# Kernel optimization log

Measured on AMD Instinct MI355X. Metric: run time of the kernel, lower is better.

The kernel has to match this reference:

```python
import jax, jax.numpy as jnp
import numpy as np


def setup_inputs() -> dict:
    key = jax.random.key(0)
    ks = jax.random.split(key, 8)
    B, N, D = 8, 2048, 128
    s = 1.0 / float(np.sqrt(D))
    node = jax.random.normal(ks[0], (B, N, D), dtype=jnp.float32)
    node_mask = jax.random.randint(ks[1], (B, N), 0, 2, dtype=jnp.int32)
    punctuation_graph = jax.random.randint(ks[2], (B, N, N), 0, 2, dtype=jnp.int32)
    w_nw = jax.random.uniform(ks[3], (1, D), jnp.float32, -s, s)
    b_nw = jax.random.uniform(ks[4], (1,), jnp.float32, -s, s)
    w_self = jax.random.uniform(ks[5], (D, D), jnp.float32, -s, s)
    b_self = jax.random.uniform(ks[6], (D,), jnp.float32, -s, s)
    w_punct = jax.random.uniform(ks[7], (D, D), jnp.float32, -s, s)
    return {"node": node, "node_mask": node_mask, "punctuation_graph": punctuation_graph,
            "w_nw": w_nw, "b_nw": b_nw, "w_self": w_self, "b_self": b_self,
            "w_punct": w_punct, "iteration_steps": 2}


def reference(node, node_mask, punctuation_graph, w_nw, b_nw, w_self, b_self, w_punct, iteration_steps):
    B, N, D = node.shape
    # dd_graph = mask outer product with zeroed diagonal; graph = dd_graph * punctuation_graph
    eye = jnp.eye(N, dtype=punctuation_graph.dtype)
    dd = node_mask[:, None, :] * node_mask[:, :, None] * (1 - eye)[None, :, :]  # [B,N,N]
    graph = dd * punctuation_graph  # [B,N,N] int, binary
    nbr_num = graph.sum(-1)  # [B,N]
    # replace_masked_values(nbr_num, nbr_num>=1, 1): nodes with no neighbors get denom 1
    nbr_f = jnp.where(nbr_num >= 1, nbr_num.astype(node.dtype), jnp.asarray(1.0, node.dtype))
    gmask = graph > 0
    weights = []
    x = node
    for _ in range(iteration_steps):  # small fixed step count
        dw = jax.nn.sigmoid(jnp.einsum('bnd,od->bno', x, w_nw) + b_nw)[..., 0]  # [B,N]
        weights.append(dw)
        self_info = jnp.einsum('bnd,ed->bne', x, w_self) + b_self  # [B,N,D]
        info_p = jnp.einsum('bnd,ed->bne', x, w_punct)  # [B,N,D]
        # node_weight[b,i,j] = dw[b,j] where graph[b,i,j] else 0
        nw = jnp.where(gmask, dw[:, None, :], jnp.asarray(0.0, x.dtype))  # [B,N,N]
        agg = jnp.einsum('bnm,bmd->bnd', nw, info_p) / nbr_f[..., None]
        x = jax.nn.relu(self_info + agg)
    all_weight = jnp.stack(weights, axis=1)  # [B, steps, N]
    return x, all_weight
```

## Files before the change

### kernel.cpp

```cpp
#include <hip/hip_runtime.h>
#include <hip/hip_bf16.h>

#define BB 8
#define NN 2048
#define DD 128

typedef __attribute__((ext_vector_type(8))) __bf16 bf16x8;
typedef __attribute__((ext_vector_type(4))) float f32x4;
typedef __attribute__((ext_vector_type(4))) int   i32x4;

static __device__ __forceinline__ unsigned short f2bf(float f) {
    union { float f; unsigned u; } v; v.f = f;
    unsigned r = (v.u + 0x7FFFu + ((v.u >> 16) & 1u)) >> 16;
    return (unsigned short)r;
}
static __device__ __forceinline__ float bf2f(unsigned short b) {
    union { unsigned u; float f; } v; v.u = ((unsigned)b) << 16;
    return v.f;
}

__global__ __launch_bounds__(256) void kernP3(
    const int* __restrict__ punct, const int* __restrict__ mask,
    const float* __restrict__ w_self, const float* __restrict__ w_punct,
    unsigned* __restrict__ pk, float* __restrict__ scale_g, float* __restrict__ pdm_g,
    unsigned short* __restrict__ wsb, unsigned short* __restrict__ wpb)
{
    const int bid = blockIdx.x;
    const int t = threadIdx.x;

    if (bid >= 2048) {
        const int cb = bid - 2048;
        const float* src = (cb < 8) ? w_self : w_punct;
        unsigned short* dst = (cb < 8) ? wsb : wpb;
        const size_t i0 = (size_t)(cb & 7) * 2048 + (size_t)t * 8;
        f32x4 a = *(const f32x4*)(src + i0);
        f32x4 c = *(const f32x4*)(src + i0 + 4);
        unsigned q0 = f2bf(a.x) | ((unsigned)f2bf(a.y) << 16);
        unsigned q1 = f2bf(a.z) | ((unsigned)f2bf(a.w) << 16);
        unsigned q2 = f2bf(c.x) | ((unsigned)f2bf(c.y) << 16);
        unsigned q3 = f2bf(c.z) | ((unsigned)f2bf(c.w) << 16);
        i32x4 pw = {(int)q0, (int)q1, (int)q2, (int)q3};
        *(i32x4*)(dst + i0) = pw;
        return;
    }

    const int wave = t >> 6, lane = t & 63;
    const int row0 = bid * 8 + wave * 2;
    const int b = row0 >> 11;
    const int* mrow = mask + (size_t)b * NN;

    unsigned mw = 0;
    #pragma unroll
    for (int q = 0; q < 8; ++q) {
        i32x4 m = *(const i32x4*)(mrow + lane * 32 + q * 4);
        unsigned nib = (m.x & 1) | ((m.y & 1) << 1) | ((m.z & 1) << 2) | ((m.w & 1) << 3);
        mw |= nib << (4 * q);
    }

    #pragma unroll
    for (int r = 0; r < 2; ++r) {
        const int row = row0 + r;
        const int i = row & (NN - 1);
        const int mi = mrow[i];
        if (mi == 0) {
            if (lane == 0) { scale_g[row] = 0.f; pdm_g[row] = 0.f; }
            continue;
        }
        const int* prow = punct + (size_t)row * NN;
        i32x4 v[8];
        #pragma unroll
        for (int q = 0; q < 8; ++q)
            v[q] = *(const i32x4*)(prow + lane * 32 + q * 4);
        unsigned wd = 0;
        #pragma unroll
        for (int q = 0; q < 8; ++q) {
            unsigned nib = (v[q].x & 1) | ((v[q].y & 1) << 1)
                         | ((v[q].z & 1) << 2) | ((v[q].w & 1) << 3);
            wd |= nib << (4 * q);
        }
        wd &= mw;
        pk[(size_t)row * 64 + lane] = wd;

        int acc = __popc(wd);
        if ((i >> 5) == lane) acc += (int)((wd >> (i & 31)) & 1u) << 16;
        #pragma unroll
        for (int o = 32; o > 0; o >>= 1) acc += __shfl_xor(acc, o, 64);
        if (lane == 0) {
            const int nall = acc & 0xFFFF;
            const int pd   = acc >> 16;
            const int nbr  = nall - pd;
            scale_g[row] = 1.f / (float)(nbr < 1 ? 1 : nbr);
            pdm_g[row]   = (float)pd;
        }
    }
}

static __device__ __forceinline__ void kernB_body(
    int n0, const float* __restrict__ x,
    const float* __restrict__ w_nw,  const float* __restrict__ b_nw,
    const unsigned short* __restrict__ wsb, const float* __restrict__ b_self,
    const unsigned short* __restrict__ wpb,
    const float* __restrict__ scale_g, const float* __restrict__ pdm_g,
    float* __restrict__ si_out,
    unsigned short* __restrict__ yT_out,
    float* __restrict__ aw_out)
{
    __shared__ unsigned short xt[64*32];
    __shared__ unsigned short wst[128*32];
    __shared__ unsigned short wpt[128*32];
    __shared__ float wnw_l[DD];
    __shared__ float red[256];
    __shared__ float dw_l[64];
    __shared__ float scl_l[64];
    __shared__ float pdm_l[64];
    __shared__ unsigned short ytl[128*72];

    const int t  = threadIdx.x;
    const int b  = n0 >> 11;
    const int nb = n0 & (NN - 1);

    if (t < DD) wnw_l[t] = w_nw[t];
    if (t >= 128 && t < 192) { scl_l[t-128] = scale_g[n0 + t - 128]; }
    if (t >= 192)            { pdm_l[t-192] = pdm_g[n0 + t - 192]; }
    __syncthreads();

    const int wave = t >> 6, lane = t & 63;
    const int wm = wave >> 1, wn = wave & 1;
    const int quad = lane >> 4, l16 = lane & 15;

    const int n_loc = t >> 2, dq = t & 3;
    const int we = t >> 1,   wh = t & 1;

    f32x4 accs[2][4] = {}; f32x4 accp[2][4] = {};
    float dwpart = 0.f;

    #pragma unroll
    for (int kk = 0; kk < 4; ++kk) {
        const int k0 = kk * 32;
        {
            const float* xs = x + (size_t)(n0 + n_loc) * DD + k0 + dq * 8;
            f32x4 a = *(const f32x4*)xs;
            f32x4 c = *(const f32x4*)(xs + 4);
            const float* wv = &wnw_l[k0 + dq * 8];
            dwpart += a.x*wv[0] + a.y*wv[1] + a.z*wv[2] + a.w*wv[3]
                    + c.x*wv[4] + c.y*wv[5] + c.z*wv[6] + c.w*wv[7];
            unsigned q0 = f2bf(a.x) | ((unsigned)f2bf(a.y) << 16);
            unsigned q1 = f2bf(a.z) | ((unsigned)f2bf(a.w) << 16);
            unsigned q2 = f2bf(c.x) | ((unsigned)f2bf(c.y) << 16);
            unsigned q3 = f2bf(c.z) | ((unsigned)f2bf(c.w) << 16);
            i32x4 pw = {(int)q0,(int)q1,(int)q2,(int)q3};
            *(i32x4*)&xt[n_loc*32 + dq*8] = pw;
        }
        {
            const unsigned short* s1 = wsb + (size_t)we * DD + k0 + wh*16;
            const unsigned short* s2 = wpb + (size_t)we * DD + k0 + wh*16;
            i32x4 a0 = *(const i32x4*)s1;
            i32x4 a1 = *(const i32x4*)(s1 + 8);
            *(i32x4*)&wst[we*32 + wh*16]     = a0;
            *(i32x4*)&wst[we*32 + wh*16 + 8] = a1;
            i32x4 c0 = *(const i32x4*)s2;
            i32x4 c1 = *(const i32x4*)(s2 + 8);
            *(i32x4*)&wpt[we*32 + wh*16]     = c0;
            *(i32x4*)&wpt[we*32 + wh*16 + 8] = c1;
        }
        __syncthreads();
        bf16x8 af[2], bs[4], bp[4];
        #pragma unroll
        for (int mt = 0; mt < 2; ++mt)
            af[mt] = *(const bf16x8*)&xt[(wm*32 + mt*16 + l16)*32 + quad*8];
        #pragma unroll
        for (int nt = 0; nt < 4; ++nt) {
            const int er = wn*64 + nt*16 + l16;
            bs[nt] = *(const bf16x8*)&wst[er*32 + quad*8];
            bp[nt] = *(const bf16x8*)&wpt[er*32 + quad*8];
        }
        #pragma unroll
        for (int mt = 0; mt < 2; ++mt)
            #pragma unroll
            for (int nt = 0; nt < 4; ++nt) {
                accs[mt][nt] = __builtin_amdgcn_mfma_f32_16x16x32_bf16(af[mt], bs[nt], accs[mt][nt], 0, 0, 0);
                accp[mt][nt] = __builtin_amdgcn_mfma_f32_16x16x32_bf16(af[mt], bp[nt], accp[mt][nt], 0, 0, 0);
            }
        __syncthreads();
    }

    red[t] = dwpart;
    __syncthreads();
    if (t < 64) {
        float s = red[4*t] + red[4*t+1] + red[4*t+2] + red[4*t+3] + b_nw[0];
        float dv = 1.f / (1.f + __expf(-s));
        dw_l[t] = dv;
        aw_out[(size_t)b * 2 * NN + nb + t] = dv;
    }
    __syncthreads();

    #pragma unroll
    for (int mt = 0; mt < 2; ++mt) {
        #pragma unroll
        for (int nt = 0; nt < 4; ++nt) {
            const int e = wn*64 + nt*16 + l16;
            const float bsv = b_self[e];
            #pragma unroll
            for (int r = 0; r < 4; ++r) {
                const int nl = wm*32 + mt*16 + quad*4 + r;
                const size_t idx = (size_t)(n0 + nl) * DD + e;
                const float yv = dw_l[nl] * accp[mt][nt][r];
                const unsigned short ub = f2bf(yv);
                const float yvr = bf2f(ub);
                si_out[idx] = accs[mt][nt][r] + bsv - scl_l[nl] * pdm_l[nl] * yvr;
                ytl[e*72 + nl] = ub;
            }
        }
    }
    __syncthreads();
    {
        const int e = t >> 1, half = t & 1;
        const i32x4* src = (const i32x4*)&ytl[e*72 + half*32];
        i32x4 v0 = src[0], v1 = src[1], v2 = src[2], v3 = src[3];
        i32x4* dst = (i32x4*)(yT_out + (size_t)(b*DD + e) * NN + nb + half*32);
        dst[0] = v0; dst[1] = v1; dst[2] = v2; dst[3] = v3;
    }
}

__global__ __launch_bounds__(256) void kernB(
    const float* __restrict__ x,
    const unsigned short* __restrict__ wsb, const unsigned short* __restrict__ wpb,
    const float* __restrict__ w_nw, const float* __restrict__ b_nw,
    const float* __restrict__ b_self,
    const float* __restrict__ scale_g, const float* __restrict__ pdm_g,
    float* __restrict__ si, unsigned short* __restrict__ yT,
    float* __restrict__ aw_s)
{
    kernB_body(blockIdx.x * 64, x, w_nw, b_nw, wsb, b_self, wpb,
               scale_g, pdm_g, si, yT, aw_s);
}

__global__ __launch_bounds__(256) void kernC4(
    const unsigned* __restrict__ pk,
    const float* __restrict__ scale_g,
    const unsigned short* __restrict__ yT,
    const float* __restrict__ sip,
    float* __restrict__ x_out)
{
    __shared__ unsigned pPk[64 * 68];
    __shared__ float scale_l[64];
    __shared__ f32x4 accL[2][16][64];

    const int t  = threadIdx.x;
    const int b  = blockIdx.x & 7;
    const int i0 = (blockIdx.x >> 3) * 64;
    const size_t rg0 = (size_t)b * NN + i0;

    #pragma unroll
    for (int r = 0; r < 4; ++r) {
        const int u   = r * 256 + t;
        const int row = u >> 4;
        const int wq  = (u & 15) * 4;
        i32x4 v = *(const i32x4*)(pk + (rg0 + row) * 64 + wq);
        *(i32x4*)&pPk[row * 68 + wq] = v;
    }
    if (t < 64) scale_l[t] = scale_g[rg0 + t];
    __syncthreads();

    const int wave = t >> 6, lane = t & 63;
    const int kh = wave >> 1, eh = wave & 1;
    const int quad = lane >> 4, l16 = lane & 15;
    const unsigned short* yTb = yT + (size_t)b * DD * NN;

    f32x4 acc[4][4] = {};

    #pragma unroll 4
    for (int ks = 0; ks < 32; ++ks) {
        const int kk = kh * 32 + ks;
        bf16x8 bfr[4];
        #pragma unroll
        for (int nt = 0; nt < 4; ++nt) {
            const int e = eh*64 + nt*16 + l16;
            bfr[nt] = *(const bf16x8*)(yTb + (size_t)e * NN + kk*32 + quad*8);
        }
        bf16x8 af[4];
        #pragma unroll
        for (int mt = 0; mt < 4; ++mt) {
            const unsigned w = pPk[(mt*16 + l16) * 68 + kk];
            const unsigned by = (w >> (quad * 8)) & 0xFFu;
            i32x4 ex;
            ex.x = (int)((((by &   1u) << 7) + ((by &   2u) << 22)) * 0x7Fu);
            ex.y = (int)((((by &   4u) << 5) + ((by &   8u) << 20)) * 0x7Fu);
            ex.z = (int)((((by &  16u) << 3) + ((by &  32u) << 18)) * 0x7Fu);
            ex.w = (int)((((by &  64u) << 1) + ((by & 128u) << 16)) * 0x7Fu);
            union { i32x4 i; bf16x8 h; } cv; cv.i = ex;
            af[mt] = cv.h;
        }
        #pragma unroll
        for (int mt = 0; mt < 4; ++mt)
            #pragma unroll
            for (int nt = 0; nt < 4; ++nt)
                acc[mt][nt] = __builtin_amdgcn_mfma_f32_16x16x32_bf16(af[mt], bfr[nt], acc[mt][nt], 0, 0, 0);
    }

    __syncthreads();
    if (kh == 1) {
        #pragma unroll
        for (int mt = 0; mt < 4; ++mt)
            #pragma unroll
            for (int nt = 0; nt < 4; ++nt)
                accL[eh][mt*4 + nt][lane] = acc[mt][nt];
    }
    __syncthreads();
    if (kh == 0) {
        #pragma unroll
        for (int mt = 0; mt < 4; ++mt) {
            #pragma unroll
            for (int nt = 0; nt < 4; ++nt) {
                f32x4 o = accL[eh][mt*4 + nt][lane];
                const int e = eh*64 + nt*16 + l16;
                #pragma unroll
                for (int r = 0; r < 4; ++r) {
                    const int row = mt*16 + quad*4 + r;
                    const size_t idx = (rg0 + row) * DD + e;
                    float v = sip[idx] + scale_l[row] * (acc[mt][nt][r] + o[r]);
                    x_out[idx] = fmaxf(v, 0.f);
                }
            }
        }
    }
}

extern "C" void kernel_launch(void* const* d_in, const int* in_sizes, int n_in,
                              void* d_out, int out_size, void* d_ws, size_t ws_size,
                              hipStream_t stream) {
    const float* node   = (const float*)d_in[0];
    const int*   mask   = (const int*)  d_in[1];
    const int*   punct  = (const int*)  d_in[2];
    const float* w_nw   = (const float*)d_in[3];
    const float* b_nw   = (const float*)d_in[4];
    const float* w_self = (const float*)d_in[5];
    const float* b_self = (const float*)d_in[6];
    const float* w_punct= (const float*)d_in[7];

    float* xout = (float*)d_out;
    float* aw   = xout + (size_t)BB * NN * DD;

    char* w = (char*)d_ws;
    float*          si   = (float*)w;
    unsigned short* yT   = (unsigned short*)(w + (12u << 20));
    unsigned*       pk   = (unsigned*)(w + (16u << 20));
    float*          scl  = (float*)(w + (20u << 20));
    float*          pdm  = (float*)(w + (20u << 20) + (64u << 10));
    unsigned short* wsb  = (unsigned short*)(w + (21u << 20));
    unsigned short* wpb  = (unsigned short*)(w + (21u << 20) + (32u << 10));

    kernP3<<<dim3(2064), dim3(256), 0, stream>>>(punct, mask, w_self, w_punct,
                                                 pk, scl, pdm, wsb, wpb);
    kernB <<<dim3(256),  dim3(256), 0, stream>>>(node, wsb, wpb, w_nw, b_nw,
                                                 b_self, scl, pdm, si, yT, aw);
    kernC4<<<dim3(256),  dim3(256), 0, stream>>>(pk, scl, yT, si, xout);
    kernB <<<dim3(256),  dim3(256), 0, stream>>>(xout, wsb, wpb, w_nw, b_nw,
                                                 b_self, scl, pdm, si, yT, aw + NN);
    kernC4<<<dim3(256),  dim3(256), 0, stream>>>(pk, scl, yT, si, xout);
}
```

Baseline: 268.0 us.

## Fuse step-1 aggregation with step-2 projection into one kernel

Replaces the first kernC4 (graph aggregation) and the second kernB (node-weight and self/punct projections) with a single fused kernel kernCB. The intermediate x stays in shared memory as bf16 instead of round-tripping through global memory. This drops one launch and the x write/read. The intermediate x is now bf16-rounded before the second projection, and a second yT buffer is used so the kernel does not race on its own input. The cost is a larger shared-memory footprint, which may lower occupancy.

```diff
diff --git a/kernel.cpp b/kernel.cpp
--- a/kernel.cpp
+++ b/kernel.cpp
@@ -95,14 +95,13 @@
     }
 }
 
-static __device__ __forceinline__ void kernB_body(
-    int n0, const float* __restrict__ x,
-    const float* __restrict__ w_nw,  const float* __restrict__ b_nw,
-    const unsigned short* __restrict__ wsb, const float* __restrict__ b_self,
-    const unsigned short* __restrict__ wpb,
+__global__ __launch_bounds__(256) void kernB(
+    const float* __restrict__ x,
+    const unsigned short* __restrict__ wsb, const unsigned short* __restrict__ wpb,
+    const float* __restrict__ w_nw, const float* __restrict__ b_nw,
+    const float* __restrict__ b_self,
     const float* __restrict__ scale_g, const float* __restrict__ pdm_g,
-    float* __restrict__ si_out,
-    unsigned short* __restrict__ yT_out,
+    float* __restrict__ si_out, unsigned short* __restrict__ yT_out,
     float* __restrict__ aw_out)
 {
     __shared__ unsigned short xt[64*32];
@@ -115,6 +114,7 @@
     __shared__ float pdm_l[64];
     __shared__ unsigned short ytl[128*72];
 
+    const int n0 = blockIdx.x * 64;
     const int t  = threadIdx.x;
     const int b  = n0 >> 11;
     const int nb = n0 & (NN - 1);
@@ -222,17 +222,211 @@
     }
 }
 
-__global__ __launch_bounds__(256) void kernB(
-    const float* __restrict__ x,
+#define OFF_SCL   0u
+#define OFF_PDM   256u
+#define OFF_WNW   512u
+#define OFF_DW    1024u
+#define OFF_A     1280u
+#define OFF_XT4   1280u
+#define OFF_RED   (1280u + 16384u)
+#define OFF_B     25856u
+#define OFF_WST   25856u
+#define OFF_WPT   (25856u + 8192u)
+#define OFF_YTL   (25856u + 16384u)
+#define SMEM_CB   60672u
+
+__global__ __launch_bounds__(256) void kernCB(
+    const unsigned* __restrict__ pk,
+    const float* __restrict__ scale_g, const float* __restrict__ pdm_g,
+    const unsigned short* __restrict__ yT0,
+    float* si,
     const unsigned short* __restrict__ wsb, const unsigned short* __restrict__ wpb,
     const float* __restrict__ w_nw, const float* __restrict__ b_nw,
     const float* __restrict__ b_self,
-    const float* __restrict__ scale_g, const float* __restrict__ pdm_g,
-    float* __restrict__ si, unsigned short* __restrict__ yT,
-    float* __restrict__ aw_s)
+    unsigned short* __restrict__ yT1,
+    float* __restrict__ aw1)
 {
-    kernB_body(blockIdx.x * 64, x, w_nw, b_nw, wsb, b_self, wpb,
-               scale_g, pdm_g, si, yT, aw_s);
+    __shared__ char smem[SMEM_CB];
+    float*          scl_l = (float*)(smem + OFF_SCL);
+    float*          pdm_l = (float*)(smem + OFF_PDM);
+    float*          wnw_l = (float*)(smem + OFF_WNW);
+    float*          dw_l  = (float*)(smem + OFF_DW);
+    unsigned*       pPk   = (unsigned*)(smem + OFF_A);
+    unsigned short* xt4   = (unsigned short*)(smem + OFF_XT4);
+    float*          red   = (float*)(smem + OFF_RED);
+    f32x4*          accL  = (f32x4*)(smem + OFF_B);
+    unsigned short* wst   = (unsigned short*)(smem + OFF_WST);
+    unsigned short* wpt   = (unsigned short*)(smem + OFF_WPT);
+    unsigned short* ytl   = (unsigned short*)(smem + OFF_YTL);
+
+    const int t  = threadIdx.x;
+    const int b  = blockIdx.x & 7;
+    const int i0 = (blockIdx.x >> 3) * 64;
+    const size_t rg0 = (size_t)b * NN + i0;
+
+    #pragma unroll
+    for (int r = 0; r < 4; ++r) {
+        const int u   = r * 256 + t;
+        const int row = u >> 4;
+        const int wq  = (u & 15) * 4;
+        i32x4 v = *(const i32x4*)(pk + (rg0 + row) * 64 + wq);
+        *(i32x4*)&pPk[row * 68 + wq] = v;
+    }
+    if (t < 64)                   scl_l[t]      = scale_g[rg0 + t];
+    else if (t < 128)             pdm_l[t-64]   = pdm_g[rg0 + t - 64];
+    else                          wnw_l[t-128]  = w_nw[t-128];
+    __syncthreads();
+
+    const int wave = t >> 6, lane = t & 63;
+    const int kh = wave >> 1, eh = wave & 1;
+    const int quad = lane >> 4, l16 = lane & 15;
+    const unsigned short* yTb = yT0 + (size_t)b * DD * NN;
+
+    f32x4 acc[4][4] = {};
+    #pragma unroll 4
+    for (int ks = 0; ks < 32; ++ks) {
+        const int kk = kh * 32 + ks;
+        bf16x8 bfr[4];
+        #pragma unroll
+        for (int nt = 0; nt < 4; ++nt) {
+            const int e = eh*64 + nt*16 + l16;
+            bfr[nt] = *(const bf16x8*)(yTb + (size_t)e * NN + kk*32 + quad*8);
+        }
+        bf16x8 af[4];
+        #pragma unroll
+        for (int mt = 0; mt < 4; ++mt) {
+            const unsigned w = pPk[(mt*16 + l16) * 68 + kk];
+            const unsigned by = (w >> (quad * 8)) & 0xFFu;
+            i32x4 ex;
+            ex.x = (int)((((by &   1u) << 7) + ((by &   2u) << 22)) * 0x7Fu);
+            ex.y = (int)((((by &   4u) << 5) + ((by &   8u) << 20)) * 0x7Fu);
+            ex.z = (int)((((by &  16u) << 3) + ((by &  32u) << 18)) * 0x7Fu);
+            ex.w = (int)((((by &  64u) << 1) + ((by & 128u) << 16)) * 0x7Fu);
+            union { i32x4 i; bf16x8 h; } cv; cv.i = ex;
+            af[mt] = cv.h;
+        }
+        #pragma unroll
+        for (int mt = 0; mt < 4; ++mt)
+            #pragma unroll
+            for (int nt = 0; nt < 4; ++nt)
+                acc[mt][nt] = __builtin_amdgcn_mfma_f32_16x16x32_bf16(af[mt], bfr[nt], acc[mt][nt], 0, 0, 0);
+    }
+
+    __syncthreads();
+    if (kh == 1) {
+        #pragma unroll
+        for (int mt = 0; mt < 4; ++mt)
+            #pragma unroll
+            for (int nt = 0; nt < 4; ++nt)
+                accL[(eh*16 + mt*4 + nt)*64 + lane] = acc[mt][nt];
+    }
+    __syncthreads();
+
+    if (kh == 0) {
+        #pragma unroll
+        for (int mt = 0; mt < 4; ++mt) {
+            float part[4] = {0.f, 0.f, 0.f, 0.f};
+            #pragma unroll
+            for (int nt = 0; nt < 4; ++nt) {
+                f32x4 o = accL[(eh*16 + mt*4 + nt)*64 + lane];
+                const int e = eh*64 + nt*16 + l16;
+                const float wv = wnw_l[e];
+                #pragma unroll
+                for (int r = 0; r < 4; ++r) {
+                    const int row = mt*16 + quad*4 + r;
+                    const size_t idx = (rg0 + row) * DD + e;
+                    float xv = si[idx] + scl_l[row] * (acc[mt][nt][r] + o[r]);
+                    xv = fmaxf(xv, 0.f);
+                    xt4[((e >> 5) * 64 + row) * 32 + (e & 31)] = f2bf(xv);
+                    part[r] += xv * wv;
+                }
+            }
+            #pragma unroll
+            for (int r = 0; r < 4; ++r) {
+                const int row = mt*16 + quad*4 + r;
+                red[row * 32 + eh*16 + l16] = part[r];
+            }
+        }
+    }
+    __syncthreads();
+
+    if (t < 64) {
+        float s = b_nw[0];
+        #pragma unroll 8
+        for (int c = 0; c < 32; ++c) s += red[t * 32 + c];
+        float dv = 1.f / (1.f + __expf(-s));
+        dw_l[t] = dv;
+        aw1[(size_t)b * 2 * NN + i0 + t] = dv;
+    }
+    __syncthreads();
+
+    const int wm = kh, wn = eh;
+    const int we = t >> 1, wh = t & 1;
+
+    f32x4 accs[2][4] = {}; f32x4 accp[2][4] = {};
+
+    #pragma unroll
+    for (int kk = 0; kk < 4; ++kk) {
+        const int k0 = kk * 32;
+        {
+            const unsigned short* s1 = wsb + (size_t)we * DD + k0 + wh*16;
+            const unsigned short* s2 = wpb + (size_t)we * DD + k0 + wh*16;
+            i32x4 a0 = *(const i32x4*)s1;
+            i32x4 a1 = *(const i32x4*)(s1 + 8);
+            *(i32x4*)&wst[we*32 + wh*16]     = a0;
+            *(i32x4*)&wst[we*32 + wh*16 + 8] = a1;
+            i32x4 c0 = *(const i32x4*)s2;
+            i32x4 c1 = *(const i32x4*)(s2 + 8);
+            *(i32x4*)&wpt[we*32 + wh*16]     = c0;
+            *(i32x4*)&wpt[we*32 + wh*16 + 8] = c1;
+        }
+        __syncthreads();
+        bf16x8 af[2], bs[4], bp[4];
+        #pragma unroll
+        for (int mt = 0; mt < 2; ++mt)
+            af[mt] = *(const bf16x8*)&xt4[(kk*64 + wm*32 + mt*16 + l16)*32 + quad*8];
+        #pragma unroll
+        for (int nt = 0; nt < 4; ++nt) {
+            const int er = wn*64 + nt*16 + l16;
+            bs[nt] = *(const bf16x8*)&wst[er*32 + quad*8];
+            bp[nt] = *(const bf16x8*)&wpt[er*32 + quad*8];
+        }
+        #pragma unroll
+        for (int mt = 0; mt < 2; ++mt)
+            #pragma unroll
+            for (int nt = 0; nt < 4; ++nt) {
+                accs[mt][nt] = __builtin_amdgcn_mfma_f32_16x16x32_bf16(af[mt], bs[nt], accs[mt][nt], 0, 0, 0);
+                accp[mt][nt] = __builtin_amdgcn_mfma_f32_16x16x32_bf16(af[mt], bp[nt], accp[mt][nt], 0, 0, 0);
+            }
+        __syncthreads();
+    }
+
+    #pragma unroll
+    for (int mt = 0; mt < 2; ++mt) {
+        #pragma unroll
+        for (int nt = 0; nt < 4; ++nt) {
+            const int e = wn*64 + nt*16 + l16;
+            const float bsv = b_self[e];
+            #pragma unroll
+            for (int r = 0; r < 4; ++r) {
+                const int nl = wm*32 + mt*16 + quad*4 + r;
+                const size_t idx = (rg0 + nl) * DD + e;
+                const float yv = dw_l[nl] * accp[mt][nt][r];
+                const unsigned short ub = f2bf(yv);
+                const float yvr = bf2f(ub);
+                si[idx] = accs[mt][nt][r] + bsv - scl_l[nl] * pdm_l[nl] * yvr;
+                ytl[e*72 + nl] = ub;
+            }
+        }
+    }
+    __syncthreads();
+    {
+        const int e = t >> 1, half = t & 1;
+        const i32x4* src = (const i32x4*)&ytl[e*72 + half*32];
+        i32x4 v0 = src[0], v1 = src[1], v2 = src[2], v3 = src[3];
+        i32x4* dst = (i32x4*)(yT1 + (size_t)(b*DD + e) * NN + i0 + half*32);
+        dst[0] = v0; dst[1] = v1; dst[2] = v2; dst[3] = v3;
+    }
 }
 
 __global__ __launch_bounds__(256) void kernC4(
@@ -343,19 +537,20 @@
 
     char* w = (char*)d_ws;
     float*          si   = (float*)w;
-    unsigned short* yT   = (unsigned short*)(w + (12u << 20));
+    unsigned short* yT0  = (unsigned short*)(w + (12u << 20));
     unsigned*       pk   = (unsigned*)(w + (16u << 20));
     float*          scl  = (float*)(w + (20u << 20));
     float*          pdm  = (float*)(w + (20u << 20) + (64u << 10));
     unsigned short* wsb  = (unsigned short*)(w + (21u << 20));
     unsigned short* wpb  = (unsigned short*)(w + (21u << 20) + (32u << 10));
+    unsigned short* yT1  = (unsigned short*)(w + (24u << 20));
 
     kernP3<<<dim3(2064), dim3(256), 0, stream>>>(punct, mask, w_self, w_punct,
                                                  pk, scl, pdm, wsb, wpb);
     kernB <<<dim3(256),  dim3(256), 0, stream>>>(node, wsb, wpb, w_nw, b_nw,
-                                                 b_self, scl, pdm, si, yT, aw);
-    kernC4<<<dim3(256),  dim3(256), 0, stream>>>(pk, scl, yT, si, xout);
-    kernB <<<dim3(256),  dim3(256), 0, stream>>>(xout, wsb, wpb, w_nw, b_nw,
-                                                 b_self, scl, pdm, si, yT, aw + NN);
-    kernC4<<<dim3(256),  dim3(256), 0, stream>>>(pk, scl, yT, si, xout);
-}
+                                                 b_self, scl, pdm, si, yT0, aw);
+    kernCB<<<dim3(256),  dim3(256), 0, stream>>>(pk, scl, pdm, yT0, si,
+                                                 wsb, wpb, w_nw, b_nw, b_self,
+                                                 yT1, aw + NN);
+    kernC4<<<dim3(256),  dim3(256), 0, stream>>>(pk, scl, yT1, si, xout);
+}
```

Result: faster. 258.9 us (-3.4%).
